# Performance work log

Hardware: AMD Instinct MI355X
Metric: run time of the kernel (lower is better)

The kernel has to match this reference:

```python
import jax, jax.numpy as jnp
import numpy as np

DIM = 1024
HEADS = 16
DIM_HEAD = 64
INNER = HEADS * DIM_HEAD  # 1024
EPS = 1e-5


def setup_inputs() -> dict:
    key = jax.random.key(0)
    ks = jax.random.split(key, 5)
    x = jax.random.normal(ks[0], (4, 2048, DIM), dtype=jnp.float32)
    ln_gamma = jnp.ones((DIM,), dtype=jnp.float32)
    ln_beta = jnp.zeros((DIM,), dtype=jnp.float32)
    # nn.Linear weights ~ U(-1/sqrt(fan_in), 1/sqrt(fan_in)); stored as (out, in) in torch,
    # here kept as (in, out) for x @ W.
    lim = 1.0 / np.sqrt(DIM)
    w_qkv = jax.random.uniform(ks[1], (DIM, 3 * INNER), minval=-lim, maxval=lim, dtype=jnp.float32)
    lim2 = 1.0 / np.sqrt(INNER)
    w_out = jax.random.uniform(ks[2], (INNER, DIM), minval=-lim2, maxval=lim2, dtype=jnp.float32)
    return {"x": x, "ln_gamma": ln_gamma, "ln_beta": ln_beta, "w_qkv": w_qkv, "w_out": w_out}


def reference(x, ln_gamma, ln_beta, w_qkv, w_out):
    b, n, d = x.shape
    # LayerNorm
    mu = jnp.mean(x, axis=-1, keepdims=True)
    var = jnp.mean(jnp.square(x - mu), axis=-1, keepdims=True)
    xn = (x - mu) * jax.lax.rsqrt(var + EPS) * ln_gamma + ln_beta
    # QKV projection
    qkv = xn @ w_qkv  # (b, n, 3*inner)
    q, k, v = jnp.split(qkv, 3, axis=-1)
    def to_heads(t):
        return t.reshape(b, n, HEADS, DIM_HEAD).transpose(0, 2, 1, 3)  # (b,h,n,dh)
    q, k, v = to_heads(q), to_heads(k), to_heads(v)
    scale = DIM_HEAD ** -0.5
    scores = jnp.einsum('bhqd,bhkd->bhqk', q, k) * scale
    causal = jnp.tril(jnp.ones((n, n), dtype=bool))
    scores = jnp.where(causal, scores, -jnp.inf)
    probs = jax.nn.softmax(scores, axis=-1)
    out = jnp.einsum('bhqk,bhkd->bhqd', probs, v)
    out = out.transpose(0, 2, 1, 3).reshape(b, n, INNER)
    return out @ w_out
```

## Files before the change

### kernel.cpp

```cpp
#include <hip/hip_runtime.h>
#include <hip/hip_bf16.h>

#define DIM 1024
#define HEADS 16
#define DH 64
#define SEQ 2048
#define BATCH 4
#define ROWS (BATCH * SEQ)
#define NQKV (3 * DIM)

typedef __attribute__((ext_vector_type(8))) __bf16 bf16x8;
typedef __attribute__((ext_vector_type(4))) __bf16 bf16x4;
typedef __attribute__((ext_vector_type(4))) float f32x4;

__device__ inline void gload16(const void* g, void* l) {
  __builtin_amdgcn_global_load_lds(
      (const __attribute__((address_space(1))) void*)g,
      (__attribute__((address_space(3))) void*)l, 16, 0, 0);
}

__device__ inline float fast_exp2(float x) {
#if __has_builtin(__builtin_amdgcn_exp2f)
  return __builtin_amdgcn_exp2f(x);
#else
  return exp2f(x);
#endif
}

__global__ __launch_bounds__(256) void ln_kernel(
    const float* __restrict__ x, const float* __restrict__ gamma,
    const float* __restrict__ beta, __bf16* __restrict__ xnb) {
  const int row = blockIdx.x;
  const int tid = threadIdx.x;
  const float4* xr = (const float4*)(x + (size_t)row * DIM);
  float4 v = xr[tid];
  float s1 = v.x + v.y + v.z + v.w;
  float s2 = v.x * v.x + v.y * v.y + v.z * v.z + v.w * v.w;
#pragma unroll
  for (int d = 32; d > 0; d >>= 1) {
    s1 += __shfl_xor(s1, d);
    s2 += __shfl_xor(s2, d);
  }
  __shared__ float red1[4], red2[4];
  const int wave = tid >> 6, lane = tid & 63;
  if (lane == 0) { red1[wave] = s1; red2[wave] = s2; }
  __syncthreads();
  s1 = red1[0] + red1[1] + red1[2] + red1[3];
  s2 = red2[0] + red2[1] + red2[2] + red2[3];
  const float mean = s1 * (1.0f / DIM);
  const float var = s2 * (1.0f / DIM) - mean * mean;
  const float rstd = rsqrtf(var + 1e-5f);
  float4 g = ((const float4*)gamma)[tid];
  float4 b = ((const float4*)beta)[tid];
  bf16x4 o;
  o[0] = (__bf16)((v.x - mean) * rstd * g.x + b.x);
  o[1] = (__bf16)((v.y - mean) * rstd * g.y + b.y);
  o[2] = (__bf16)((v.z - mean) * rstd * g.z + b.z);
  o[3] = (__bf16)((v.w - mean) * rstd * g.w + b.w);
  *(bf16x4*)(xnb + (size_t)row * DIM + tid * 4) = o;
}

__global__ __launch_bounds__(256) void transpose_cast2(
    const float* __restrict__ wq, const float* __restrict__ wo,
    __bf16* __restrict__ qT, __bf16* __restrict__ oT) {
  __shared__ float tile[32][33];
  const int tx = threadIdx.x & 31, ty = threadIdx.x >> 5;
  int bx = blockIdx.x;
  const float* in;
  __bf16* out;
  int cols;
  if (bx < 96) {
    in = wq; out = qT; cols = NQKV;
  } else {
    in = wo; out = oT; cols = DIM; bx -= 96;
  }
  const int c0 = bx * 32, r0 = blockIdx.y * 32;
#pragma unroll
  for (int rr = ty; rr < 32; rr += 8)
    tile[rr][tx] = in[(size_t)(r0 + rr) * cols + c0 + tx];
  __syncthreads();
#pragma unroll
  for (int rr = ty; rr < 32; rr += 8)
    out[(size_t)(c0 + rr) * DIM + r0 + tx] = (__bf16)tile[tx][rr];
}

template <int MODE>
__global__ __launch_bounds__(512, 1) void gemmP(
    const __bf16* __restrict__ A, const __bf16* __restrict__ Bt, const int K,
    const int N, float* __restrict__ Cout, __bf16* __restrict__ qb,
    __bf16* __restrict__ kb, __bf16* __restrict__ vtb) {
  __shared__ __bf16 As[3][2][128 * 64];
  __shared__ __bf16 Bs[3][128 * 64];
  const int tid = threadIdx.x;
  const int wave = tid >> 6, lane = tid & 63;
  const int quad = lane >> 4, l16 = lane & 15;
  const int wm = wave >> 2, wn = wave & 3;

  const size_t tileM = (size_t)blockIdx.x * 256;
  const size_t tileN = (size_t)blockIdx.y * 128;
  const int sel = (MODE == 1) ? (int)(tileN >> 10) : 0;
  const bool vmode = (MODE == 1) && (sel == 2);

  f32x4 acc[8][2];
#pragma unroll
  for (int i = 0; i < 8; ++i)
#pragma unroll
    for (int j = 0; j < 2; ++j) acc[i][j] = (f32x4){0.f, 0.f, 0.f, 0.f};

  const __bf16* Abase = A + tileM * (size_t)K;
  const __bf16* Bbase = Bt + tileN * (size_t)K;

  const int slr = tid >> 3, sc = tid & 7;
  const int scol = (sc ^ (slr & 7)) << 3;

  auto stageA = [&](int buf, int h, int kt) {
    const size_t col = (size_t)(kt << 6) + scol;
#pragma unroll
    for (int p = 0; p < 2; ++p) {
      const int gr = p * 128 + h * 64 + slr;
      const int lr = p * 64 + slr;
      gload16(Abase + (size_t)gr * K + col, &As[buf][h][lr * 64 + sc * 8]);
    }
  };
  auto stageB = [&](int buf, int kt) {
    const size_t col = (size_t)(kt << 6) + scol;
#pragma unroll
    for (int p = 0; p < 2; ++p) {
      const int lr = p * 64 + slr;
      gload16(Bbase + (size_t)lr * K + col, &Bs[buf][lr * 64 + sc * 8]);
    }
  };
  auto stageTile = [&](int buf, int kt) {
    stageA(buf, 0, kt);
    stageB(buf, kt);
    stageA(buf, 1, kt);
  };

  const int rpc = quad ^ (l16 & 7);
  auto ldA = [&](int buf, int mt, int ks) -> bf16x8 {
    const int lr = wm * 64 + (mt & 3) * 16 + l16;
    return *(const bf16x8*)&As[buf][mt >> 2][lr * 64 + ((rpc ^ (ks << 2)) << 3)];
  };
  auto ldB = [&](int buf, int nt, int ks) -> bf16x8 {
    const int lr = wn * 32 + nt * 16 + l16;
    return *(const bf16x8*)&Bs[buf][lr * 64 + ((rpc ^ (ks << 2)) << 3)];
  };

  auto cluster = [&](const bf16x8* af, bf16x8 bf0, bf16x8 bf1, int mb) {
    __builtin_amdgcn_s_setprio(1);
    if (vmode) {
#pragma unroll
      for (int mt = 0; mt < 4; ++mt) {
        acc[mb + mt][0] = __builtin_amdgcn_mfma_f32_16x16x32_bf16(
            af[mt], bf0, acc[mb + mt][0], 0, 0, 0);
        acc[mb + mt][1] = __builtin_amdgcn_mfma_f32_16x16x32_bf16(
            af[mt], bf1, acc[mb + mt][1], 0, 0, 0);
      }
    } else {
#pragma unroll
      for (int mt = 0; mt < 4; ++mt) {
        acc[mb + mt][0] = __builtin_amdgcn_mfma_f32_16x16x32_bf16(
            bf0, af[mt], acc[mb + mt][0], 0, 0, 0);
        acc[mb + mt][1] = __builtin_amdgcn_mfma_f32_16x16x32_bf16(
            bf1, af[mt], acc[mb + mt][1], 0, 0, 0);
      }
    }
    __builtin_amdgcn_s_setprio(0);
  };

  stageTile(0, 0);
  stageTile(1, 1);

  const int NT = K >> 6;
  int bufc = 0;
  bf16x8 af[4], b00, b01, b10, b11;

  for (int t = 0; t < NT; ++t) {
    if (t < NT - 1)
      asm volatile("s_waitcnt vmcnt(6)" ::: "memory");
    else
      asm volatile("s_waitcnt vmcnt(0)" ::: "memory");
    __builtin_amdgcn_s_barrier();
    asm volatile("" ::: "memory");
    __builtin_amdgcn_sched_barrier(0);

    if (t + 2 < NT) {
      const int sb = bufc + 2 >= 3 ? bufc - 1 : bufc + 2;
      stageTile(sb, t + 2);
    }

#pragma unroll
    for (int mt = 0; mt < 4; ++mt) af[mt] = ldA(bufc, mt, 0);
    b00 = ldB(bufc, 0, 0);
    b01 = ldB(bufc, 1, 0);
    cluster(af, b00, b01, 0);
#pragma unroll
    for (int mt = 0; mt < 4; ++mt) af[mt] = ldA(bufc, mt, 1);
    b10 = ldB(bufc, 0, 1);
    b11 = ldB(bufc, 1, 1);
    cluster(af, b10, b11, 0);
#pragma unroll
    for (int mt = 0; mt < 4; ++mt) af[mt] = ldA(bufc, 4 + mt, 0);
    cluster(af, b00, b01, 4);
#pragma unroll
    for (int mt = 0; mt < 4; ++mt) af[mt] = ldA(bufc, 4 + mt, 1);
    cluster(af, b10, b11, 4);

    bufc = bufc == 2 ? 0 : bufc + 1;
  }

  if (MODE == 0) {
#pragma unroll
    for (int mt = 0; mt < 8; ++mt) {
      const size_t m = tileM + wm * 128 + mt * 16 + l16;
#pragma unroll
      for (int nt = 0; nt < 2; ++nt) {
        const size_t n0 = tileN + wn * 32 + nt * 16 + quad * 4;
        *(f32x4*)&Cout[m * (size_t)N + n0] = acc[mt][nt];
      }
    }
  } else if (sel < 2) {
    __bf16* dst = (sel == 0) ? qb : kb;
#pragma unroll
    for (int mt = 0; mt < 8; ++mt) {
      const size_t m = tileM + wm * 128 + mt * 16 + l16;
      const int b = (int)(m >> 11), seq = (int)(m & 2047);
#pragma unroll
      for (int nt = 0; nt < 2; ++nt) {
        const int c = (int)(tileN & 1023) + wn * 32 + nt * 16 + quad * 4;
        const int head = c >> 6, dh = c & 63;
        bf16x4 pk;
#pragma unroll
        for (int r = 0; r < 4; ++r) pk[r] = (__bf16)acc[mt][nt][r];
        *(bf16x4*)&dst[(((size_t)b * HEADS + head) * SEQ + seq) * DH + dh] = pk;
      }
    }
  } else {
#pragma unroll
    for (int nt = 0; nt < 2; ++nt) {
      const int c = (int)(tileN & 1023) + wn * 32 + nt * 16 + l16;
      const int head = c >> 6, dh = c & 63;
#pragma unroll
      for (int mt = 0; mt < 8; ++mt) {
        const size_t m0 = tileM + wm * 128 + mt * 16 + quad * 4;
        const int b = (int)(m0 >> 11), seq = (int)(m0 & 2047);
        bf16x4 pk;
#pragma unroll
        for (int r = 0; r < 4; ++r) pk[r] = (__bf16)acc[mt][nt][r];
        *(bf16x4*)&vtb[(((size_t)b * HEADS + head) * DH + dh) * SEQ + seq] = pk;
      }
    }
  }
}

__global__ __launch_bounds__(256, 4) void attn_kernel(
    const __bf16* __restrict__ qb, const __bf16* __restrict__ kb,
    const __bf16* __restrict__ vtb, __bf16* __restrict__ ob) {
  const int bh = blockIdx.x;
  const int by = blockIdx.y;
  const int tid = threadIdx.x;
  const int wave = tid >> 6, lane = tid & 63;
  const int quad = lane >> 4, l16 = lane & 15;

  __shared__ __bf16 Ks[2][64 * 64];
  __shared__ __bf16 Vs[2][64 * 64];
  __shared__ __bf16 Ps[4][16 * 36];

  const __bf16* kg = kb + (size_t)bh * SEQ * DH;
  const __bf16* vg = vtb + (size_t)bh * DH * SEQ;

  const int i1 = by, i2 = 31 - by;
  const int T = 33;

  const int kr = lane >> 3, kc = lane & 7;

  auto stage = [&](int buf, int j) {
#pragma unroll
    for (int p = 0; p < 2; ++p) {
      const int rbase = wave * 16 + p * 8;
      const int row = rbase + kr;
      gload16(kg + (size_t)(j * 64 + row) * DH + ((kc ^ (row & 7)) << 3),
              &Ks[buf][rbase * 64]);
      gload16(vg + (size_t)row * SEQ + j * 64 + ((kc ^ (row & 7)) << 3),
              &Vs[buf][rbase * 64]);
    }
  };

  const float QSCALE = 0.125f * 1.44269504088896f;
  bf16x8 qf[2];
  auto load_q = [&](int i) {
    const __bf16* qbase = qb + ((size_t)bh * SEQ + (size_t)i * 64 + wave * 16) * DH;
#pragma unroll
    for (int ks = 0; ks < 2; ++ks) {
      bf16x8 v = *(const bf16x8*)(qbase + l16 * DH + ks * 32 + quad * 8);
#pragma unroll
      for (int e = 0; e < 8; ++e) v[e] = (__bf16)((float)v[e] * QSCALE);
      qf[ks] = v;
    }
  };

  float m_i, l_i;
  f32x4 o_acc[4];
  auto reset_state = [&]() {
    m_i = -1e30f;
    l_i = 0.f;
#pragma unroll
    for (int md = 0; md < 4; ++md) o_acc[md] = (f32x4){0.f, 0.f, 0.f, 0.f};
  };
  const int b_out = bh >> 4, h_out = bh & 15;
  auto epilogue = [&](int i) {
    float lsum = l_i;
    lsum += __shfl_xor(lsum, 16);
    lsum += __shfl_xor(lsum, 32);
    const float inv = __builtin_amdgcn_rcpf(lsum);
    const int seq = i * 64 + wave * 16 + l16;
    __bf16* dst = ob + ((size_t)b_out * SEQ + seq) * DIM + h_out * DH;
#pragma unroll
    for (int md = 0; md < 4; ++md) {
      bf16x4 pk;
#pragma unroll
      for (int r = 0; r < 4; ++r) pk[r] = (__bf16)(o_acc[md][r] * inv);
      *(bf16x4*)(dst + md * 16 + quad * 4) = pk;
    }
  };

  load_q(i1);
  reset_state();
  stage(0, 0);

  for (int t = 0; t < T; ++t) {
    __syncthreads();
    if (t + 1 < T) {
      const int jn = (t + 1 <= by) ? (t + 1) : (t - by);
      stage((t + 1) & 1, jn);
    }
    const int buf = t & 1;
    const int i = (t <= by) ? i1 : i2;
    const int j = (t <= by) ? t : (t - by - 1);
    const bool diag = (j == i);

    f32x4 sa[4];
#pragma unroll
    for (int nt = 0; nt < 4; ++nt) sa[nt] = (f32x4){0.f, 0.f, 0.f, 0.f};
#pragma unroll
    for (int nt = 0; nt < 4; ++nt)
#pragma unroll
      for (int ks = 0; ks < 2; ++ks) {
        bf16x8 kf = *(const bf16x8*)&Ks[buf][(nt * 16 + l16) * 64 +
                                            (((ks * 4 + quad) ^ (l16 & 7)) << 3)];
        sa[nt] = __builtin_amdgcn_mfma_f32_16x16x32_bf16(kf, qf[ks], sa[nt], 0, 0, 0);
      }

    if (diag) {
      const int qrl = wave * 16 + l16;
#pragma unroll
      for (int nt = 0; nt < 4; ++nt)
#pragma unroll
        for (int r = 0; r < 4; ++r) {
          const int kvl = nt * 16 + quad * 4 + r;
          if (kvl > qrl) sa[nt][r] = -1e30f;
        }
    }

    {
      float mx = -1e30f;
#pragma unroll
      for (int nt = 0; nt < 4; ++nt) {
        const float a0 = fmaxf(fmaxf(sa[nt][0], sa[nt][1]), sa[nt][2]);
        mx = fmaxf(mx, fmaxf(a0, sa[nt][3]));
      }
      mx = fmaxf(mx, __shfl_xor(mx, 16));
      mx = fmaxf(mx, __shfl_xor(mx, 32));
      if (__all(mx - m_i <= 8.f)) {
        float rs = 0.f;
#pragma unroll
        for (int nt = 0; nt < 4; ++nt)
#pragma unroll
          for (int r = 0; r < 4; ++r) {
            const float p = fast_exp2(sa[nt][r] - m_i);
            sa[nt][r] = p;
            rs += p;
          }
        l_i += rs;
      } else {
        const float mnew = fmaxf(m_i, mx);
        const float alpha = fast_exp2(m_i - mnew);
        m_i = mnew;
        float rs = 0.f;
#pragma unroll
        for (int nt = 0; nt < 4; ++nt)
#pragma unroll
          for (int r = 0; r < 4; ++r) {
            const float p = fast_exp2(sa[nt][r] - mnew);
            sa[nt][r] = p;
            rs += p;
          }
        l_i = l_i * alpha + rs;
#pragma unroll
        for (int md = 0; md < 4; ++md)
#pragma unroll
          for (int r = 0; r < 4; ++r) o_acc[md][r] *= alpha;
      }
    }

#pragma unroll
    for (int c = 0; c < 2; ++c) {
#pragma unroll
      for (int ntl = 0; ntl < 2; ++ntl) {
        const int nt = c * 2 + ntl;
        bf16x4 pk;
#pragma unroll
        for (int r = 0; r < 4; ++r) pk[r] = (__bf16)sa[nt][r];
        *(bf16x4*)&Ps[wave][l16 * 36 + ntl * 16 + quad * 4] = pk;
      }
      bf16x8 pf = *(const bf16x8*)&Ps[wave][l16 * 36 + quad * 8];
#pragma unroll
      for (int md = 0; md < 4; ++md) {
        bf16x8 vf = *(const bf16x8*)&Vs[buf][(md * 16 + l16) * 64 +
                                            (((c * 4 + quad) ^ (l16 & 7)) << 3)];
        o_acc[md] = __builtin_amdgcn_mfma_f32_16x16x32_bf16(vf, pf, o_acc[md], 0, 0, 0);
      }
    }

    if (t == by) {
      epilogue(i1);
      reset_state();
      load_q(i2);
    }
  }
  epilogue(i2);
}

extern "C" void kernel_launch(void* const* d_in, const int* in_sizes, int n_in,
                              void* d_out, int out_size, void* d_ws, size_t ws_size,
                              hipStream_t stream) {
  const float* x = (const float*)d_in[0];
  const float* gamma = (const float*)d_in[1];
  const float* beta = (const float*)d_in[2];
  const float* w_qkv = (const float*)d_in[3];
  const float* w_out = (const float*)d_in[4];
  float* out = (float*)d_out;

  char* ws = (char*)d_ws;
  const size_t MB = 1024 * 1024;
  __bf16* xnb = (__bf16*)ws;
  __bf16* wqkvT = (__bf16*)(ws + 16 * MB);
  __bf16* woutT = (__bf16*)(ws + 24 * MB);
  __bf16* qbuf = (__bf16*)(ws + 32 * MB);
  __bf16* kbuf = (__bf16*)(ws + 48 * MB);
  __bf16* vtbuf = (__bf16*)(ws + 64 * MB);
  __bf16* attnb = xnb;

  ln_kernel<<<ROWS, 256, 0, stream>>>(x, gamma, beta, xnb);
  transpose_cast2<<<dim3(128, 32), 256, 0, stream>>>(w_qkv, w_out, wqkvT, woutT);
  gemmP<1><<<dim3(ROWS / 256, NQKV / 128), 512, 0, stream>>>(
      xnb, wqkvT, DIM, NQKV, nullptr, qbuf, kbuf, vtbuf);
  attn_kernel<<<dim3(BATCH * HEADS, 16), 256, 0, stream>>>(qbuf, kbuf, vtbuf, attnb);
  gemmP<0><<<dim3(ROWS / 256, DIM / 128), 512, 0, stream>>>(
      attnb, woutT, DIM, DIM, out, nullptr, nullptr, nullptr);
}
```

Baseline: 271.7 us.

## Widen GEMM tiles to 256x256 with double-buffered interleaved staging

```diff
diff --git a/kernel.cpp b/kernel.cpp
--- a/kernel.cpp
+++ b/kernel.cpp
@@ -26,6 +26,13 @@
   return exp2f(x);
 #endif
 }
+
+#define BARRIER_FENCE()                      \
+  do {                                       \
+    __builtin_amdgcn_s_barrier();            \
+    asm volatile("" ::: "memory");           \
+    __builtin_amdgcn_sched_barrier(0);       \
+  } while (0)
 
 __global__ __launch_bounds__(256) void ln_kernel(
     const float* __restrict__ x, const float* __restrict__ gamma,
@@ -85,27 +92,27 @@
 }
 
 template <int MODE>
-__global__ __launch_bounds__(512, 1) void gemmP(
+__global__ __launch_bounds__(512, 1) void gemm256(
     const __bf16* __restrict__ A, const __bf16* __restrict__ Bt, const int K,
     const int N, float* __restrict__ Cout, __bf16* __restrict__ qb,
     __bf16* __restrict__ kb, __bf16* __restrict__ vtb) {
-  __shared__ __bf16 As[3][2][128 * 64];
-  __shared__ __bf16 Bs[3][128 * 64];
+  __shared__ __bf16 As[2][2][128 * 64];
+  __shared__ __bf16 Bs[2][256 * 64];
   const int tid = threadIdx.x;
   const int wave = tid >> 6, lane = tid & 63;
   const int quad = lane >> 4, l16 = lane & 15;
   const int wm = wave >> 2, wn = wave & 3;
 
   const size_t tileM = (size_t)blockIdx.x * 256;
-  const size_t tileN = (size_t)blockIdx.y * 128;
+  const size_t tileN = (size_t)blockIdx.y * 256;
   const int sel = (MODE == 1) ? (int)(tileN >> 10) : 0;
   const bool vmode = (MODE == 1) && (sel == 2);
 
-  f32x4 acc[8][2];
+  f32x4 acc[8][4];
 #pragma unroll
   for (int i = 0; i < 8; ++i)
 #pragma unroll
-    for (int j = 0; j < 2; ++j) acc[i][j] = (f32x4){0.f, 0.f, 0.f, 0.f};
+    for (int j = 0; j < 4; ++j) acc[i][j] = (f32x4){0.f, 0.f, 0.f, 0.f};
 
   const __bf16* Abase = A + tileM * (size_t)K;
   const __bf16* Bbase = Bt + tileN * (size_t)K;
@@ -113,7 +120,15 @@
   const int slr = tid >> 3, sc = tid & 7;
   const int scol = (sc ^ (slr & 7)) << 3;
 
-  auto stageA = [&](int buf, int h, int kt) {
+  auto stageB2 = [&](int buf, int kt, int pp) {
+    const size_t col = (size_t)(kt << 6) + scol;
+#pragma unroll
+    for (int p = 0; p < 2; ++p) {
+      const int row = pp * 128 + p * 64 + slr;
+      gload16(Bbase + (size_t)row * K + col, &Bs[buf][row * 64 + sc * 8]);
+    }
+  };
+  auto stageAh = [&](int buf, int kt, int h) {
     const size_t col = (size_t)(kt << 6) + scol;
 #pragma unroll
     for (int p = 0; p < 2; ++p) {
@@ -122,19 +137,6 @@
       gload16(Abase + (size_t)gr * K + col, &As[buf][h][lr * 64 + sc * 8]);
     }
   };
-  auto stageB = [&](int buf, int kt) {
-    const size_t col = (size_t)(kt << 6) + scol;
-#pragma unroll
-    for (int p = 0; p < 2; ++p) {
-      const int lr = p * 64 + slr;
-      gload16(Bbase + (size_t)lr * K + col, &Bs[buf][lr * 64 + sc * 8]);
-    }
-  };
-  auto stageTile = [&](int buf, int kt) {
-    stageA(buf, 0, kt);
-    stageB(buf, kt);
-    stageA(buf, 1, kt);
-  };
 
   const int rpc = quad ^ (l16 & 7);
   auto ldA = [&](int buf, int mt, int ks) -> bf16x8 {
@@ -142,71 +144,77 @@
     return *(const bf16x8*)&As[buf][mt >> 2][lr * 64 + ((rpc ^ (ks << 2)) << 3)];
   };
   auto ldB = [&](int buf, int nt, int ks) -> bf16x8 {
-    const int lr = wn * 32 + nt * 16 + l16;
+    const int lr = wn * 64 + nt * 16 + l16;
     return *(const bf16x8*)&Bs[buf][lr * 64 + ((rpc ^ (ks << 2)) << 3)];
   };
 
-  auto cluster = [&](const bf16x8* af, bf16x8 bf0, bf16x8 bf1, int mb) {
+  auto cluster16 = [&](const bf16x8* af, const bf16x8* bf, int mb) {
     __builtin_amdgcn_s_setprio(1);
     if (vmode) {
 #pragma unroll
-      for (int mt = 0; mt < 4; ++mt) {
-        acc[mb + mt][0] = __builtin_amdgcn_mfma_f32_16x16x32_bf16(
-            af[mt], bf0, acc[mb + mt][0], 0, 0, 0);
-        acc[mb + mt][1] = __builtin_amdgcn_mfma_f32_16x16x32_bf16(
-            af[mt], bf1, acc[mb + mt][1], 0, 0, 0);
-      }
+      for (int mt = 0; mt < 4; ++mt)
+#pragma unroll
+        for (int nt = 0; nt < 4; ++nt)
+          acc[mb + mt][nt] = __builtin_amdgcn_mfma_f32_16x16x32_bf16(
+              af[mt], bf[nt], acc[mb + mt][nt], 0, 0, 0);
     } else {
 #pragma unroll
-      for (int mt = 0; mt < 4; ++mt) {
-        acc[mb + mt][0] = __builtin_amdgcn_mfma_f32_16x16x32_bf16(
-            bf0, af[mt], acc[mb + mt][0], 0, 0, 0);
-        acc[mb + mt][1] = __builtin_amdgcn_mfma_f32_16x16x32_bf16(
-            bf1, af[mt], acc[mb + mt][1], 0, 0, 0);
-      }
+      for (int mt = 0; mt < 4; ++mt)
+#pragma unroll
+        for (int nt = 0; nt < 4; ++nt)
+          acc[mb + mt][nt] = __builtin_amdgcn_mfma_f32_16x16x32_bf16(
+              bf[nt], af[mt], acc[mb + mt][nt], 0, 0, 0);
     }
     __builtin_amdgcn_s_setprio(0);
   };
 
-  stageTile(0, 0);
-  stageTile(1, 1);
+  stageB2(0, 0, 0);
+  stageB2(0, 0, 1);
+  stageAh(0, 0, 0);
+  stageAh(0, 0, 1);
 
   const int NT = K >> 6;
-  int bufc = 0;
-  bf16x8 af[4], b00, b01, b10, b11;
+  bf16x8 af[4], bk0[4], bk1[4];
 
   for (int t = 0; t < NT; ++t) {
-    if (t < NT - 1)
-      asm volatile("s_waitcnt vmcnt(6)" ::: "memory");
+    const int buf = t & 1, nbuf = buf ^ 1;
+    const bool st = (t + 1 < NT);
+    asm volatile("s_waitcnt vmcnt(2)" ::: "memory");
+    BARRIER_FENCE();
+
+#pragma unroll
+    for (int mt = 0; mt < 4; ++mt) af[mt] = ldA(buf, mt, 0);
+#pragma unroll
+    for (int nt = 0; nt < 4; ++nt) bk0[nt] = ldB(buf, nt, 0);
+    if (st) stageB2(nbuf, t + 1, 0);
+    BARRIER_FENCE();
+
+    cluster16(af, bk0, 0);
+#pragma unroll
+    for (int mt = 0; mt < 4; ++mt) af[mt] = ldA(buf, mt, 1);
+#pragma unroll
+    for (int nt = 0; nt < 4; ++nt) bk1[nt] = ldB(buf, nt, 1);
+    if (st) stageB2(nbuf, t + 1, 1);
+    BARRIER_FENCE();
+
+    cluster16(af, bk1, 0);
+    if (st)
+      asm volatile("s_waitcnt vmcnt(4)" ::: "memory");
     else
       asm volatile("s_waitcnt vmcnt(0)" ::: "memory");
-    __builtin_amdgcn_s_barrier();
-    asm volatile("" ::: "memory");
     __builtin_amdgcn_sched_barrier(0);
-
-    if (t + 2 < NT) {
-      const int sb = bufc + 2 >= 3 ? bufc - 1 : bufc + 2;
-      stageTile(sb, t + 2);
-    }
-
-#pragma unroll
-    for (int mt = 0; mt < 4; ++mt) af[mt] = ldA(bufc, mt, 0);
-    b00 = ldB(bufc, 0, 0);
-    b01 = ldB(bufc, 1, 0);
-    cluster(af, b00, b01, 0);
-#pragma unroll
-    for (int mt = 0; mt < 4; ++mt) af[mt] = ldA(bufc, mt, 1);
-    b10 = ldB(bufc, 0, 1);
-    b11 = ldB(bufc, 1, 1);
-    cluster(af, b10, b11, 0);
-#pragma unroll
-    for (int mt = 0; mt < 4; ++mt) af[mt] = ldA(bufc, 4 + mt, 0);
-    cluster(af, b00, b01, 4);
-#pragma unroll
-    for (int mt = 0; mt < 4; ++mt) af[mt] = ldA(bufc, 4 + mt, 1);
-    cluster(af, b10, b11, 4);
-
-    bufc = bufc == 2 ? 0 : bufc + 1;
+#pragma unroll
+    for (int mt = 0; mt < 4; ++mt) af[mt] = ldA(buf, 4 + mt, 0);
+    if (st) stageAh(nbuf, t + 1, 0);
+    BARRIER_FENCE();
+
+    cluster16(af, bk0, 4);
+#pragma unroll
+    for (int mt = 0; mt < 4; ++mt) af[mt] = ldA(buf, 4 + mt, 1);
+    if (st) stageAh(nbuf, t + 1, 1);
+    BARRIER_FENCE();
+
+    cluster16(af, bk1, 4);
   }
 
   if (MODE == 0) {
@@ -214,8 +222,8 @@
     for (int mt = 0; mt < 8; ++mt) {
       const size_t m = tileM + wm * 128 + mt * 16 + l16;
 #pragma unroll
-      for (int nt = 0; nt < 2; ++nt) {
-        const size_t n0 = tileN + wn * 32 + nt * 16 + quad * 4;
+      for (int nt = 0; nt < 4; ++nt) {
+        const size_t n0 = tileN + wn * 64 + nt * 16 + quad * 4;
         *(f32x4*)&Cout[m * (size_t)N + n0] = acc[mt][nt];
       }
     }
@@ -226,8 +234,8 @@
       const size_t m = tileM + wm * 128 + mt * 16 + l16;
       const int b = (int)(m >> 11), seq = (int)(m & 2047);
 #pragma unroll
-      for (int nt = 0; nt < 2; ++nt) {
-        const int c = (int)(tileN & 1023) + wn * 32 + nt * 16 + quad * 4;
+      for (int nt = 0; nt < 4; ++nt) {
+        const int c = (int)(tileN & 1023) + wn * 64 + nt * 16 + quad * 4;
         const int head = c >> 6, dh = c & 63;
         bf16x4 pk;
 #pragma unroll
@@ -237,8 +245,8 @@
     }
   } else {
 #pragma unroll
-    for (int nt = 0; nt < 2; ++nt) {
-      const int c = (int)(tileN & 1023) + wn * 32 + nt * 16 + l16;
+    for (int nt = 0; nt < 4; ++nt) {
+      const int c = (int)(tileN & 1023) + wn * 64 + nt * 16 + l16;
       const int head = c >> 6, dh = c & 63;
 #pragma unroll
       for (int mt = 0; mt < 8; ++mt) {
@@ -453,9 +461,9 @@
 
   ln_kernel<<<ROWS, 256, 0, stream>>>(x, gamma, beta, xnb);
   transpose_cast2<<<dim3(128, 32), 256, 0, stream>>>(w_qkv, w_out, wqkvT, woutT);
-  gemmP<1><<<dim3(ROWS / 256, NQKV / 128), 512, 0, stream>>>(
+  gemm256<1><<<dim3(ROWS / 256, NQKV / 256), 512, 0, stream>>>(
       xnb, wqkvT, DIM, NQKV, nullptr, qbuf, kbuf, vtbuf);
   attn_kernel<<<dim3(BATCH * HEADS, 16), 256, 0, stream>>>(qbuf, kbuf, vtbuf, attnb);
-  gemmP<0><<<dim3(ROWS / 256, DIM / 128), 512, 0, stream>>>(
+  gemm256<0><<<dim3(ROWS / 256, DIM / 256), 512, 0, stream>>>(
       attnb, woutT, DIM, DIM, out, nullptr, nullptr, nullptr);
 }
```

Measured after the change: 329.6 us. 21.3% more time.

## Halve GEMM K-tile to 32 and shrink LDS to allow multiple blocks per CU

Applied to the files above, without the earlier changes.

```diff
diff --git a/kernel.cpp b/kernel.cpp
--- a/kernel.cpp
+++ b/kernel.cpp
@@ -85,12 +85,12 @@
 }
 
 template <int MODE>
-__global__ __launch_bounds__(512, 1) void gemmP(
+__global__ __launch_bounds__(512, 4) void gemmQ(
     const __bf16* __restrict__ A, const __bf16* __restrict__ Bt, const int K,
     const int N, float* __restrict__ Cout, __bf16* __restrict__ qb,
     __bf16* __restrict__ kb, __bf16* __restrict__ vtb) {
-  __shared__ __bf16 As[3][2][128 * 64];
-  __shared__ __bf16 Bs[3][128 * 64];
+  __shared__ __bf16 As[3][256 * 32];
+  __shared__ __bf16 Bs[3][128 * 32];
   const int tid = threadIdx.x;
   const int wave = tid >> 6, lane = tid & 63;
   const int quad = lane >> 4, l16 = lane & 15;
@@ -110,59 +110,52 @@
   const __bf16* Abase = A + tileM * (size_t)K;
   const __bf16* Bbase = Bt + tileN * (size_t)K;
 
-  const int slr = tid >> 3, sc = tid & 7;
-  const int scol = (sc ^ (slr & 7)) << 3;
-
-  auto stageA = [&](int buf, int h, int kt) {
-    const size_t col = (size_t)(kt << 6) + scol;
+  const int sr = lane >> 2;
+  const int sc = lane & 3;
+  const int ck = (l16 >> 1) & 3;
+
+  auto stageTile = [&](int buf, int kt) {
+    const int k0 = kt << 5;
 #pragma unroll
     for (int p = 0; p < 2; ++p) {
-      const int gr = p * 128 + h * 64 + slr;
-      const int lr = p * 64 + slr;
-      gload16(Abase + (size_t)gr * K + col, &As[buf][h][lr * 64 + sc * 8]);
-    }
-  };
-  auto stageB = [&](int buf, int kt) {
-    const size_t col = (size_t)(kt << 6) + scol;
-#pragma unroll
-    for (int p = 0; p < 2; ++p) {
-      const int lr = p * 64 + slr;
-      gload16(Bbase + (size_t)lr * K + col, &Bs[buf][lr * 64 + sc * 8]);
-    }
-  };
-  auto stageTile = [&](int buf, int kt) {
-    stageA(buf, 0, kt);
-    stageB(buf, kt);
-    stageA(buf, 1, kt);
-  };
-
-  const int rpc = quad ^ (l16 & 7);
-  auto ldA = [&](int buf, int mt, int ks) -> bf16x8 {
-    const int lr = wm * 64 + (mt & 3) * 16 + l16;
-    return *(const bf16x8*)&As[buf][mt >> 2][lr * 64 + ((rpc ^ (ks << 2)) << 3)];
-  };
-  auto ldB = [&](int buf, int nt, int ks) -> bf16x8 {
-    const int lr = wn * 32 + nt * 16 + l16;
-    return *(const bf16x8*)&Bs[buf][lr * 64 + ((rpc ^ (ks << 2)) << 3)];
-  };
-
-  auto cluster = [&](const bf16x8* af, bf16x8 bf0, bf16x8 bf1, int mb) {
+      const int rbase = p * 128 + wave * 16;
+      const int row = rbase + sr;
+      const int gc = (sc ^ ((row >> 1) & 3)) << 3;
+      gload16(Abase + (size_t)row * K + k0 + gc, &As[buf][rbase * 32]);
+    }
+    {
+      const int rbase = wave * 16;
+      const int row = rbase + sr;
+      const int gc = (sc ^ ((row >> 1) & 3)) << 3;
+      gload16(Bbase + (size_t)row * K + k0 + gc, &Bs[buf][rbase * 32]);
+    }
+  };
+
+  const int coff = (quad ^ ck) << 3;
+  auto ldA = [&](int buf, int mt) -> bf16x8 {
+    return *(const bf16x8*)&As[buf][(wm * 128 + mt * 16 + l16) * 32 + coff];
+  };
+  auto ldB = [&](int buf, int nt) -> bf16x8 {
+    return *(const bf16x8*)&Bs[buf][(wn * 32 + nt * 16 + l16) * 32 + coff];
+  };
+
+  auto cluster8 = [&](const bf16x8* af, bf16x8 b0, bf16x8 b1, int mb) {
     __builtin_amdgcn_s_setprio(1);
     if (vmode) {
 #pragma unroll
       for (int mt = 0; mt < 4; ++mt) {
         acc[mb + mt][0] = __builtin_amdgcn_mfma_f32_16x16x32_bf16(
-            af[mt], bf0, acc[mb + mt][0], 0, 0, 0);
+            af[mt], b0, acc[mb + mt][0], 0, 0, 0);
         acc[mb + mt][1] = __builtin_amdgcn_mfma_f32_16x16x32_bf16(
-            af[mt], bf1, acc[mb + mt][1], 0, 0, 0);
+            af[mt], b1, acc[mb + mt][1], 0, 0, 0);
       }
     } else {
 #pragma unroll
       for (int mt = 0; mt < 4; ++mt) {
         acc[mb + mt][0] = __builtin_amdgcn_mfma_f32_16x16x32_bf16(
-            bf0, af[mt], acc[mb + mt][0], 0, 0, 0);
+            b0, af[mt], acc[mb + mt][0], 0, 0, 0);
         acc[mb + mt][1] = __builtin_amdgcn_mfma_f32_16x16x32_bf16(
-            bf1, af[mt], acc[mb + mt][1], 0, 0, 0);
+            b1, af[mt], acc[mb + mt][1], 0, 0, 0);
       }
     }
     __builtin_amdgcn_s_setprio(0);
@@ -171,13 +164,13 @@
   stageTile(0, 0);
   stageTile(1, 1);
 
-  const int NT = K >> 6;
-  int bufc = 0;
-  bf16x8 af[4], b00, b01, b10, b11;
+  const int NT = K >> 5;
+  bf16x8 af[4], b0, b1;
 
   for (int t = 0; t < NT; ++t) {
+    const int buf = t % 3;
     if (t < NT - 1)
-      asm volatile("s_waitcnt vmcnt(6)" ::: "memory");
+      asm volatile("s_waitcnt vmcnt(3)" ::: "memory");
     else
       asm volatile("s_waitcnt vmcnt(0)" ::: "memory");
     __builtin_amdgcn_s_barrier();
@@ -185,28 +178,18 @@
     __builtin_amdgcn_sched_barrier(0);
 
     if (t + 2 < NT) {
-      const int sb = bufc + 2 >= 3 ? bufc - 1 : bufc + 2;
+      const int sb = buf + 2 >= 3 ? buf - 1 : buf + 2;
       stageTile(sb, t + 2);
     }
 
 #pragma unroll
-    for (int mt = 0; mt < 4; ++mt) af[mt] = ldA(bufc, mt, 0);
-    b00 = ldB(bufc, 0, 0);
-    b01 = ldB(bufc, 1, 0);
-    cluster(af, b00, b01, 0);
-#pragma unroll
-    for (int mt = 0; mt < 4; ++mt) af[mt] = ldA(bufc, mt, 1);
-    b10 = ldB(bufc, 0, 1);
-    b11 = ldB(bufc, 1, 1);
-    cluster(af, b10, b11, 0);
-#pragma unroll
-    for (int mt = 0; mt < 4; ++mt) af[mt] = ldA(bufc, 4 + mt, 0);
-    cluster(af, b00, b01, 4);
-#pragma unroll
-    for (int mt = 0; mt < 4; ++mt) af[mt] = ldA(bufc, 4 + mt, 1);
-    cluster(af, b10, b11, 4);
-
-    bufc = bufc == 2 ? 0 : bufc + 1;
+    for (int mt = 0; mt < 4; ++mt) af[mt] = ldA(buf, mt);
+    b0 = ldB(buf, 0);
+    b1 = ldB(buf, 1);
+    cluster8(af, b0, b1, 0);
+#pragma unroll
+    for (int mt = 0; mt < 4; ++mt) af[mt] = ldA(buf, 4 + mt);
+    cluster8(af, b0, b1, 4);
   }
 
   if (MODE == 0) {
@@ -453,9 +436,9 @@
 
   ln_kernel<<<ROWS, 256, 0, stream>>>(x, gamma, beta, xnb);
   transpose_cast2<<<dim3(128, 32), 256, 0, stream>>>(w_qkv, w_out, wqkvT, woutT);
-  gemmP<1><<<dim3(ROWS / 256, NQKV / 128), 512, 0, stream>>>(
+  gemmQ<1><<<dim3(ROWS / 256, NQKV / 128), 512, 0, stream>>>(
       xnb, wqkvT, DIM, NQKV, nullptr, qbuf, kbuf, vtbuf);
   attn_kernel<<<dim3(BATCH * HEADS, 16), 256, 0, stream>>>(qbuf, kbuf, vtbuf, attnb);
-  gemmP<0><<<dim3(ROWS / 256, DIM / 128), 512, 0, stream>>>(
+  gemmQ<0><<<dim3(ROWS / 256, DIM / 128), 512, 0, stream>>>(
       attnb, woutT, DIM, DIM, out, nullptr, nullptr, nullptr);
 }
```

Result: slower. 294.7 us (+8.5%).
